# Kernel tuning notes

Hardware: AMD Instinct MI355X
Metric: run time of the kernel (lower is better)

## Reference

```python
import jax, jax.numpy as jnp
import numpy as np

B, N, X, Y, W1, W2 = 2, 6, 8, 8, 8, 8
DIM, HEADS, DHEAD = 128, 4, 32
HD = HEADS * DHEAD
EPS = 1e-5


def setup_inputs() -> dict:
    key = jax.random.key(0)
    ks = jax.random.split(key, 12)
    d = {}
    d['q'] = jax.random.normal(ks[0], (B, N, X, Y, W1, W2, DIM), jnp.float32)
    d['k'] = jax.random.normal(ks[1], (B, N, X, Y, W1, W2, DIM), jnp.float32)
    d['v'] = jax.random.normal(ks[2], (B, N, X, Y, W1, W2, DIM), jnp.float32)
    d['skip'] = jax.random.normal(ks[3], (B, X, Y, W1, W2, DIM), jnp.float32)
    d['head_gate'] = jax.random.uniform(ks[4], (HEADS,), jnp.float32, 0.5, 1.5)
    # LayerNorm affine params (slightly perturbed so grads are nontrivial)
    d['ln_q_w'] = 1.0 + 0.1 * jax.random.normal(ks[5], (DIM,), jnp.float32)
    d['ln_q_b'] = jnp.zeros((DIM,), jnp.float32)
    d['ln_k_w'] = 1.0 + 0.1 * jax.random.normal(ks[6], (DIM,), jnp.float32)
    d['ln_k_b'] = jnp.zeros((DIM,), jnp.float32)
    d['ln_v_w'] = 1.0 + 0.1 * jax.random.normal(ks[7], (DIM,), jnp.float32)
    d['ln_v_b'] = jnp.zeros((DIM,), jnp.float32)
    # Linear weights, stored as (in, out) so x @ w + b
    s = 0.02
    d['wq'] = s * jax.random.normal(ks[8], (DIM, HD), jnp.float32)
    d['bq'] = jnp.zeros((HD,), jnp.float32)
    d['wk'] = s * jax.random.normal(ks[9], (DIM, HD), jnp.float32)
    d['bk'] = jnp.zeros((HD,), jnp.float32)
    d['wv'] = s * jax.random.normal(ks[10], (DIM, HD), jnp.float32)
    d['bv'] = jnp.zeros((HD,), jnp.float32)
    d['wp'] = s * jax.random.normal(ks[11], (HD, DIM), jnp.float32)
    d['bp'] = jnp.zeros((DIM,), jnp.float32)
    return d


def _ln(x, w, b):
    mu = jnp.mean(x, axis=-1, keepdims=True)
    var = jnp.mean(jnp.square(x - mu), axis=-1, keepdims=True)
    return (x - mu) * jax.lax.rsqrt(var + EPS) * w + b


def _windows(t):
    # (b, n, x, y, w1, w2, d) -> (b, x*y, n*w1*w2, d)
    b, n, x, y, w1, w2, dd = t.shape
    return t.transpose(0, 2, 3, 1, 4, 5, 6).reshape(b, x * y, n * w1 * w2, dd)


def _heads(t):
    # (b, l, t, HEADS*DHEAD) -> (b, m, l, t, DHEAD)
    b, l, tt, _ = t.shape
    return t.reshape(b, l, tt, HEADS, DHEAD).transpose(0, 3, 1, 2, 4)


def reference(q, k, v, skip, head_gate,
              ln_q_w, ln_q_b, ln_k_w, ln_k_b, ln_v_w, ln_v_b,
              wq, bq, wk, bk, wv, bv, wp, bp):
    b, n, x, y, w1, w2, _ = q.shape
    scale = DHEAD ** -0.5
    qh = _heads(_ln(_windows(q), ln_q_w, ln_q_b) @ wq + bq) * scale
    kh = _heads(_ln(_windows(k), ln_k_w, ln_k_b) @ wk + bk)
    vh = _heads(_ln(_windows(v), ln_v_w, ln_v_b) @ wv + bv)
    # per-window attention: l = x*y windows, Q = K = n*w1*w2 tokens
    dot = jnp.einsum('bmlqd,bmlkd->bmlqk', qh, kh)
    dot = dot * head_gate[None, :, None, None, None]
    att = jax.nn.softmax(dot, axis=-1)
    a = jnp.einsum('bmlqk,bmlkd->bmlqd', att, vh)
    a = a.transpose(0, 2, 3, 1, 4).reshape(b, x * y, n * w1 * w2, HD)
    out = a.reshape(b, x, y, n, w1, w2, HD).transpose(0, 3, 1, 2, 4, 5, 6)
    z = out @ wp + bp          # (b, n, x, y, w1, w2, dim)
    z = jnp.mean(z, axis=1)    # mean over agents n
    return z + skip
```

## Files before the change

### kernel.cpp

```cpp
#include <hip/hip_runtime.h>
#include <hip/hip_bf16.h>
#include <cstddef>

#define NB     2
#define NA     6
#define NWIN   64
#define NTOK   384
#define DIM    128
#define NHEADS 4
#define DHEAD  32

typedef __attribute__((ext_vector_type(8))) short short8;
typedef __attribute__((ext_vector_type(4))) float f32x4;

__device__ __forceinline__ unsigned short f2bf(float f) {
    __hip_bfloat16 h = __float2bfloat16(f);
    return *reinterpret_cast<unsigned short*>(&h);
}
__device__ __forceinline__ float bf2f(unsigned short u) {
    union { unsigned int i; float f; } x; x.i = ((unsigned int)u) << 16; return x.f;
}

__global__ __launch_bounds__(256) void wconv_kernel(
    const float* __restrict__ wq, const float* __restrict__ wk,
    const float* __restrict__ wv, const float* __restrict__ gate,
    unsigned short* __restrict__ wt)
{
    const int e = blockIdx.x * 256 + threadIdx.x;
    const int mat = e >> 14, i = e & 16383;
    const int kk = i >> 7, c = i & 127;
    const float* src = (mat == 0) ? wq : (mat == 1) ? wk : wv;
    const float s = (mat == 0) ? (0.17677669529663687f * gate[c >> 5]) : 1.0f;
    wt[(mat << 14) + c * DIM + kk] = f2bf(src[i] * s);
}

__global__ __launch_bounds__(256, 4) void proj_kernel(
    const float* __restrict__ qx, const float* __restrict__ kx,
    const float* __restrict__ vx,
    const float* __restrict__ lnqw, const float* __restrict__ lnqb,
    const float* __restrict__ lnkw, const float* __restrict__ lnkb,
    const float* __restrict__ lnvw, const float* __restrict__ lnvb,
    const float* __restrict__ bq, const float* __restrict__ bk,
    const float* __restrict__ bv, const float* __restrict__ gate,
    const unsigned short* __restrict__ wt,
    unsigned short* __restrict__ qh, unsigned short* __restrict__ kh,
    unsigned short* __restrict__ vh)
{
    __shared__ unsigned short Wl[DIM * DIM];

    const int bid  = blockIdx.x;
    const int mode = bid / 768;
    const int rr   = bid - mode * 768;
    const int b = rr / 384, l = (rr / 6) % NWIN, n = rr % 6;

    const float* xin  = (mode == 0) ? qx : (mode == 1) ? kx : vx;
    const float* lw   = (mode == 0) ? lnqw : (mode == 1) ? lnkw : lnvw;
    const float* lb   = (mode == 0) ? lnqb : (mode == 1) ? lnkb : lnvb;
    const float* bias = (mode == 0) ? bq : (mode == 1) ? bk : bv;
    const unsigned short* wtm = wt + (mode << 14);
    unsigned short* outp = (mode == 0) ? qh : (mode == 1) ? kh : vh;

#pragma unroll
    for (int it = 0; it < 8; ++it) {
        const int e = it * 256 + threadIdx.x;
        const int col = e >> 4, k8 = (e & 15) * 8;
        *(short8*)&Wl[col * DIM + (k8 ^ ((col & 7) << 3))] =
            *(const short8*)&wtm[col * DIM + k8];
    }

    const int wv_ = threadIdx.x >> 6, lane = threadIdx.x & 63;
    const int g = lane >> 4, qc = lane & 15;
    const int T0 = wv_ * 16;

    const float* xp = xin + ((size_t)((b * NA + n) * NWIN + l) * 64 + T0 + qc) * DIM;
    float xv[4][8];
    float s = 0.f, s2 = 0.f;
#pragma unroll
    for (int c = 0; c < 4; ++c) {
        const float4 a0 = *(const float4*)(xp + c * 32 + 8 * g);
        const float4 a1 = *(const float4*)(xp + c * 32 + 8 * g + 4);
        xv[c][0] = a0.x; xv[c][1] = a0.y; xv[c][2] = a0.z; xv[c][3] = a0.w;
        xv[c][4] = a1.x; xv[c][5] = a1.y; xv[c][6] = a1.z; xv[c][7] = a1.w;
#pragma unroll
        for (int u = 0; u < 8; ++u) { s += xv[c][u]; s2 += xv[c][u] * xv[c][u]; }
    }
    s  += __shfl_xor(s, 16);  s  += __shfl_xor(s, 32);
    s2 += __shfl_xor(s2, 16); s2 += __shfl_xor(s2, 32);
    const float mu   = s * (1.0f / 128.0f);
    const float var  = s2 * (1.0f / 128.0f) - mu * mu;
    const float rsig = rsqrtf(var + 1e-5f);

    short8 af[4];
#pragma unroll
    for (int c = 0; c < 4; ++c) {
        const float4 w0 = *(const float4*)(lw + c * 32 + 8 * g);
        const float4 w1 = *(const float4*)(lw + c * 32 + 8 * g + 4);
        const float4 b0 = *(const float4*)(lb + c * 32 + 8 * g);
        const float4 b1 = *(const float4*)(lb + c * 32 + 8 * g + 4);
        af[c][0] = (short)f2bf((xv[c][0] - mu) * rsig * w0.x + b0.x);
        af[c][1] = (short)f2bf((xv[c][1] - mu) * rsig * w0.y + b0.y);
        af[c][2] = (short)f2bf((xv[c][2] - mu) * rsig * w0.z + b0.z);
        af[c][3] = (short)f2bf((xv[c][3] - mu) * rsig * w0.w + b0.w);
        af[c][4] = (short)f2bf((xv[c][4] - mu) * rsig * w1.x + b1.x);
        af[c][5] = (short)f2bf((xv[c][5] - mu) * rsig * w1.y + b1.y);
        af[c][6] = (short)f2bf((xv[c][6] - mu) * rsig * w1.z + b1.z);
        af[c][7] = (short)f2bf((xv[c][7] - mu) * rsig * w1.w + b1.w);
    }
    __syncthreads();

    const f32x4 z = {0.f, 0.f, 0.f, 0.f};
    const float gs = 0.17677669529663687f;
    const int swz = (qc & 7) << 3;

#pragma unroll
    for (int ct = 0; ct < 8; ++ct) {
        const int col = ct * 16 + qc;
        short8 wf[4];
#pragma unroll
        for (int c = 0; c < 4; ++c)
            wf[c] = *(const short8*)&Wl[col * DIM + ((c * 32 + 8 * g) ^ swz)];

        f32x4 acc = z;
        if (mode == 2) {
#pragma unroll
            for (int c = 0; c < 4; ++c)
                acc = __builtin_amdgcn_mfma_f32_16x16x32_bf16(af[c], wf[c], acc, 0, 0, 0);
            const int head = ct >> 1;
            const int d = (ct & 1) * 16 + qc;
            const float bb = bias[col];
            const size_t hb = (size_t)(b * NHEADS + head) * NWIN + l;
            ushort4 o;
            o.x = f2bf(acc[0] + bb); o.y = f2bf(acc[1] + bb);
            o.z = f2bf(acc[2] + bb); o.w = f2bf(acc[3] + bb);
            *(ushort4*)&outp[(hb * DHEAD + d) * NTOK + n * 64 + T0 + 4 * g] = o;
        } else {
#pragma unroll
            for (int c = 0; c < 4; ++c)
                acc = __builtin_amdgcn_mfma_f32_16x16x32_bf16(wf[c], af[c], acc, 0, 0, 0);
            const int head = ct >> 1;
            const int d0 = (ct & 1) * 16 + 4 * g;
            const float hs = (mode == 0) ? (gs * gate[head]) : 1.0f;
            const float4 b4 = *(const float4*)&bias[ct * 16 + 4 * g];
            const size_t hb = (size_t)(b * NHEADS + head) * NWIN + l;
            const int t = n * 64 + T0 + qc;
            ushort4 o;
            o.x = f2bf(acc[0] + b4.x * hs); o.y = f2bf(acc[1] + b4.y * hs);
            o.z = f2bf(acc[2] + b4.z * hs); o.w = f2bf(acc[3] + b4.w * hs);
            *(ushort4*)&outp[(hb * NTOK + t) * DHEAD + d0] = o;
        }
    }
}

__global__ __launch_bounds__(256) void attn_kernel(
    const unsigned short* __restrict__ qh, const unsigned short* __restrict__ kh,
    const unsigned short* __restrict__ vt, unsigned short* __restrict__ aout)
{
    __shared__ unsigned short P[4][3][16][40];

    const int tid  = threadIdx.x;
    const int w    = tid >> 6;
    const int lane = tid & 63;
    const int g    = lane >> 4;
    const int qc   = lane & 15;

    const int idx = blockIdx.x;
    const int b = idx >> 9, h = (idx >> 7) & 3, l = (idx >> 1) & 63, half = idx & 1;
    const size_t base = (size_t)((b * NHEADS + h) * NWIN + l) * (NTOK * DHEAD);
    const unsigned short* Qp = qh + base;
    const unsigned short* Kp = kh + base;
    const unsigned short* Vp = vt + base;

    short8 qf[3];
#pragma unroll
    for (int j = 0; j < 3; ++j)
        qf[j] = *(const short8*)(Qp + (size_t)(((half * 4 + w) * 3 + j) * 16 + qc) * DHEAD + 8 * g);

    f32x4 o0[3], o1[3];
    float psum[3];
    const f32x4 z = {0.f, 0.f, 0.f, 0.f};
#pragma unroll
    for (int j = 0; j < 3; ++j) { o0[j] = z; o1[j] = z; psum[j] = 0.f; }

    for (int kc = 0; kc < 12; ++kc) {
        const int k0 = kc * 32;
        const short8 ka0 = *(const short8*)(Kp + (size_t)(k0 + qc) * DHEAD + 8 * g);
        const short8 ka1 = *(const short8*)(Kp + (size_t)(k0 + 16 + qc) * DHEAD + 8 * g);
        const short8 vb0 = *(const short8*)(Vp + (size_t)qc * NTOK + k0 + 8 * g);
        const short8 vb1 = *(const short8*)(Vp + (size_t)(16 + qc) * NTOK + k0 + 8 * g);

#pragma unroll
        for (int j = 0; j < 3; ++j) {
            f32x4 s0 = __builtin_amdgcn_mfma_f32_16x16x32_bf16(ka0, qf[j], z, 0, 0, 0);
            f32x4 s1 = __builtin_amdgcn_mfma_f32_16x16x32_bf16(ka1, qf[j], z, 0, 0, 0);
            const float e0 = __expf(s0[0]), e1 = __expf(s0[1]), e2 = __expf(s0[2]), e3 = __expf(s0[3]);
            const float e4 = __expf(s1[0]), e5 = __expf(s1[1]), e6 = __expf(s1[2]), e7 = __expf(s1[3]);
            psum[j] += ((e0 + e1) + (e2 + e3)) + ((e4 + e5) + (e6 + e7));
            ushort4 pw0, pw1;
            pw0.x = f2bf(e0); pw0.y = f2bf(e1); pw0.z = f2bf(e2); pw0.w = f2bf(e3);
            pw1.x = f2bf(e4); pw1.y = f2bf(e5); pw1.z = f2bf(e6); pw1.w = f2bf(e7);
            *(ushort4*)&P[w][j][qc][4 * g]      = pw0;
            *(ushort4*)&P[w][j][qc][16 + 4 * g] = pw1;
        }
#pragma unroll
        for (int j = 0; j < 3; ++j) {
            const short8 pa = *(const short8*)&P[w][j][qc][8 * g];
            o0[j] = __builtin_amdgcn_mfma_f32_16x16x32_bf16(pa, vb0, o0[j], 0, 0, 0);
            o1[j] = __builtin_amdgcn_mfma_f32_16x16x32_bf16(pa, vb1, o1[j], 0, 0, 0);
        }
    }

#pragma unroll
    for (int j = 0; j < 3; ++j) {
        float ps = psum[j];
        ps += __shfl_xor(ps, 16);
        ps += __shfl_xor(ps, 32);
        const float inv = 1.0f / ps;
        const int q0 = ((half * 4 + w) * 3 + j) * 16;
        const size_t ob = ((size_t)(b * NWIN + l) * NTOK + q0) * (NHEADS * DHEAD) + h * DHEAD + qc;
#pragma unroll
        for (int r = 0; r < 4; ++r) {
            const float iv = __shfl(inv, 4 * g + r);
            aout[ob + (size_t)(4 * g + r) * (NHEADS * DHEAD)]      = f2bf(o0[j][r] * iv);
            aout[ob + (size_t)(4 * g + r) * (NHEADS * DHEAD) + 16] = f2bf(o1[j][r] * iv);
        }
    }
}

__global__ __launch_bounds__(256) void outproj_kernel(
    const unsigned short* __restrict__ a, const float* __restrict__ wp,
    const float* __restrict__ bp, const float* __restrict__ skip,
    float* __restrict__ outp)
{
    __shared__ float at[DIM * 68];
    __shared__ float wl[DIM * 64];

    const int tid = threadIdx.x;
    const int bid = blockIdx.x;
    const int b = bid >> 7, l = (bid >> 1) & 63, cg = bid & 1;
    const int c0 = cg * 64;

#pragma unroll
    for (int rep = 0; rep < 8; ++rep) {
        const int idx = rep * 256 + tid;
        const int row = idx >> 4, cc4 = idx & 15;
        *(float4*)&wl[row * 64 + cc4 * 4] = *(const float4*)&wp[row * 128 + c0 + cc4 * 4];
    }

    const size_t abase = (size_t)(b * NWIN + l) * NTOK * DIM;
#pragma unroll
    for (int r = 0; r < 32; ++r) {
        const int f = tid + 256 * r;
        const int w_ = f >> 7, d = f & 127;
        float s = 0.f;
#pragma unroll
        for (int n = 0; n < NA; ++n)
            s += bf2f(a[abase + (size_t)(n * 64 + w_) * DIM + d]);
        at[d * 68 + w_] = s * (1.0f / 6.0f);
    }
    __syncthreads();

    const int cx = tid & 15, ty = tid >> 4;
    float acc[4][4];
#pragma unroll
    for (int i = 0; i < 4; ++i)
#pragma unroll
        for (int j = 0; j < 4; ++j) acc[i][j] = 0.f;

#pragma unroll 4
    for (int i = 0; i < DIM; ++i) {
        const float4 wa = *(const float4*)&wl[i * 64 + 4 * cx];
        const float4 aa = *(const float4*)&at[i * 68 + 4 * ty];
        acc[0][0] += aa.x * wa.x; acc[0][1] += aa.x * wa.y; acc[0][2] += aa.x * wa.z; acc[0][3] += aa.x * wa.w;
        acc[1][0] += aa.y * wa.x; acc[1][1] += aa.y * wa.y; acc[1][2] += aa.y * wa.z; acc[1][3] += aa.y * wa.w;
        acc[2][0] += aa.z * wa.x; acc[2][1] += aa.z * wa.y; acc[2][2] += aa.z * wa.z; acc[2][3] += aa.z * wa.w;
        acc[3][0] += aa.w * wa.x; acc[3][1] += aa.w * wa.y; acc[3][2] += aa.w * wa.z; acc[3][3] += aa.w * wa.w;
    }

    const float4 bb = *(const float4*)&bp[c0 + 4 * cx];
#pragma unroll
    for (int u = 0; u < 4; ++u) {
        const int w_ = 4 * ty + u;
        const size_t oidx = ((size_t)(b * NWIN + l) * 64 + w_) * DIM + c0 + 4 * cx;
        const float4 sk = *(const float4*)&skip[oidx];
        float4 o;
        o.x = acc[u][0] + bb.x + sk.x;
        o.y = acc[u][1] + bb.y + sk.y;
        o.z = acc[u][2] + bb.z + sk.z;
        o.w = acc[u][3] + bb.w + sk.w;
        *(float4*)&outp[oidx] = o;
    }
}

extern "C" void kernel_launch(void* const* d_in, const int* in_sizes, int n_in,
                              void* d_out, int out_size, void* d_ws, size_t ws_size,
                              hipStream_t stream) {
    const float* q      = (const float*)d_in[0];
    const float* k      = (const float*)d_in[1];
    const float* v      = (const float*)d_in[2];
    const float* skip   = (const float*)d_in[3];
    const float* gate   = (const float*)d_in[4];
    const float* ln_q_w = (const float*)d_in[5];
    const float* ln_q_b = (const float*)d_in[6];
    const float* ln_k_w = (const float*)d_in[7];
    const float* ln_k_b = (const float*)d_in[8];
    const float* ln_v_w = (const float*)d_in[9];
    const float* ln_v_b = (const float*)d_in[10];
    const float* wq     = (const float*)d_in[11];
    const float* bq     = (const float*)d_in[12];
    const float* wk     = (const float*)d_in[13];
    const float* bk     = (const float*)d_in[14];
    const float* wv     = (const float*)d_in[15];
    const float* bv     = (const float*)d_in[16];
    const float* wp     = (const float*)d_in[17];
    const float* bp     = (const float*)d_in[18];
    float* outp = (float*)d_out;

    const size_t per = (size_t)NB * NHEADS * NWIN * NTOK * DHEAD;
    unsigned short* qh = (unsigned short*)d_ws;
    unsigned short* kh = qh + per;
    unsigned short* vh = kh + per;
    unsigned short* wt = vh + per;
    unsigned short* a  = wt + 3 * 16384;

    wconv_kernel<<<192, 256, 0, stream>>>(wq, wk, wv, gate, wt);
    proj_kernel<<<3 * NB * NWIN * NA, 256, 0, stream>>>(
        q, k, v, ln_q_w, ln_q_b, ln_k_w, ln_k_b, ln_v_w, ln_v_b,
        bq, bk, bv, gate, wt, qh, kh, vh);
    attn_kernel<<<NB * NHEADS * NWIN * 2, 256, 0, stream>>>(qh, kh, vh, a);
    outproj_kernel<<<NB * NWIN * 2, 256, 0, stream>>>(a, wp, bp, skip, outp);
}
```

Before: 80.61 us.

## Fold LayerNorm affine into projection weights and apply normalization post-GEMM

Folds the LayerNorm scale into the bf16 weight matrix and precomputes per-column sums of the weights against the LN weight and bias, so the projection runs on raw bf16 inputs. Mean and inverse std are applied after the MFMA as r*(acc - mu*s_c) + t_c. The proj kernel also grows to 384 threads, with each wave handling two 16-token tiles, which cuts the block count from 2304 to 768 and spreads each weight tile load over more rows. It adds a small wsum kernel. Feeding the unnormalized x into bf16 loses precision when the mean is large relative to the spread, and the subtraction after accumulation can cancel.

```diff
diff --git a/kernel.cpp b/kernel.cpp
--- a/kernel.cpp
+++ b/kernel.cpp
@@ -23,93 +23,126 @@
 
 __global__ __launch_bounds__(256) void wconv_kernel(
     const float* __restrict__ wq, const float* __restrict__ wk,
-    const float* __restrict__ wv, const float* __restrict__ gate,
+    const float* __restrict__ wv,
+    const float* __restrict__ lnqw, const float* __restrict__ lnkw,
+    const float* __restrict__ lnvw, const float* __restrict__ gate,
     unsigned short* __restrict__ wt)
 {
     const int e = blockIdx.x * 256 + threadIdx.x;
     const int mat = e >> 14, i = e & 16383;
     const int kk = i >> 7, c = i & 127;
     const float* src = (mat == 0) ? wq : (mat == 1) ? wk : wv;
+    const float* lnw = (mat == 0) ? lnqw : (mat == 1) ? lnkw : lnvw;
     const float s = (mat == 0) ? (0.17677669529663687f * gate[c >> 5]) : 1.0f;
-    wt[(mat << 14) + c * DIM + kk] = f2bf(src[i] * s);
-}
-
-__global__ __launch_bounds__(256, 4) void proj_kernel(
-    const float* __restrict__ qx, const float* __restrict__ kx,
-    const float* __restrict__ vx,
-    const float* __restrict__ lnqw, const float* __restrict__ lnqb,
-    const float* __restrict__ lnkw, const float* __restrict__ lnkb,
-    const float* __restrict__ lnvw, const float* __restrict__ lnvb,
+    wt[(mat << 14) + c * DIM + kk] = f2bf(src[i] * lnw[kk] * s);
+}
+
+__global__ __launch_bounds__(128) void wsum_kernel(
+    const float* __restrict__ wq, const float* __restrict__ wk,
+    const float* __restrict__ wv,
+    const float* __restrict__ lnqw, const float* __restrict__ lnkw,
+    const float* __restrict__ lnvw,
+    const float* __restrict__ lnqb, const float* __restrict__ lnkb,
+    const float* __restrict__ lnvb,
     const float* __restrict__ bq, const float* __restrict__ bk,
     const float* __restrict__ bv, const float* __restrict__ gate,
-    const unsigned short* __restrict__ wt,
-    unsigned short* __restrict__ qh, unsigned short* __restrict__ kh,
-    unsigned short* __restrict__ vh)
-{
-    __shared__ unsigned short Wl[DIM * DIM];
-
-    const int bid  = blockIdx.x;
-    const int mode = bid / 768;
-    const int rr   = bid - mode * 768;
-    const int b = rr / 384, l = (rr / 6) % NWIN, n = rr % 6;
-
-    const float* xin  = (mode == 0) ? qx : (mode == 1) ? kx : vx;
-    const float* lw   = (mode == 0) ? lnqw : (mode == 1) ? lnkw : lnvw;
-    const float* lb   = (mode == 0) ? lnqb : (mode == 1) ? lnkb : lnvb;
-    const float* bias = (mode == 0) ? bq : (mode == 1) ? bk : bv;
-    const unsigned short* wtm = wt + (mode << 14);
-    unsigned short* outp = (mode == 0) ? qh : (mode == 1) ? kh : vh;
-
-#pragma unroll
-    for (int it = 0; it < 8; ++it) {
-        const int e = it * 256 + threadIdx.x;
-        const int col = e >> 4, k8 = (e & 15) * 8;
-        *(short8*)&Wl[col * DIM + (k8 ^ ((col & 7) << 3))] =
-            *(const short8*)&wtm[col * DIM + k8];
-    }
-
-    const int wv_ = threadIdx.x >> 6, lane = threadIdx.x & 63;
-    const int g = lane >> 4, qc = lane & 15;
-    const int T0 = wv_ * 16;
-
-    const float* xp = xin + ((size_t)((b * NA + n) * NWIN + l) * 64 + T0 + qc) * DIM;
-    float xv[4][8];
+    float* __restrict__ scol, float* __restrict__ tcol)
+{
+    const int mat = blockIdx.x, c = threadIdx.x;
+    const float* src  = (mat == 0) ? wq : (mat == 1) ? wk : wv;
+    const float* lnw  = (mat == 0) ? lnqw : (mat == 1) ? lnkw : lnvw;
+    const float* lnb  = (mat == 0) ? lnqb : (mat == 1) ? lnkb : lnvb;
+    const float* bias = (mat == 0) ? bq : (mat == 1) ? bk : bv;
+    float s = 0.f, t = 0.f;
+    for (int k = 0; k < DIM; ++k) {
+        const float w = src[k * DIM + c];
+        s += lnw[k] * w;
+        t += lnb[k] * w;
+    }
+    const float qs = (mat == 0) ? (0.17677669529663687f * gate[c >> 5]) : 1.0f;
+    scol[mat * DIM + c] = s * qs;
+    tcol[mat * DIM + c] = (t + bias[c]) * qs;
+}
+
+__device__ __forceinline__ void load_unit(
+    const float* __restrict__ xp, int g, short8* __restrict__ af,
+    float& mu, float& rsig)
+{
     float s = 0.f, s2 = 0.f;
 #pragma unroll
     for (int c = 0; c < 4; ++c) {
         const float4 a0 = *(const float4*)(xp + c * 32 + 8 * g);
         const float4 a1 = *(const float4*)(xp + c * 32 + 8 * g + 4);
-        xv[c][0] = a0.x; xv[c][1] = a0.y; xv[c][2] = a0.z; xv[c][3] = a0.w;
-        xv[c][4] = a1.x; xv[c][5] = a1.y; xv[c][6] = a1.z; xv[c][7] = a1.w;
-#pragma unroll
-        for (int u = 0; u < 8; ++u) { s += xv[c][u]; s2 += xv[c][u] * xv[c][u]; }
+        short8 o;
+        o[0] = (short)f2bf(a0.x); o[1] = (short)f2bf(a0.y);
+        o[2] = (short)f2bf(a0.z); o[3] = (short)f2bf(a0.w);
+        o[4] = (short)f2bf(a1.x); o[5] = (short)f2bf(a1.y);
+        o[6] = (short)f2bf(a1.z); o[7] = (short)f2bf(a1.w);
+        af[c] = o;
+        s  += ((a0.x + a0.y) + (a0.z + a0.w)) + ((a1.x + a1.y) + (a1.z + a1.w));
+        s2 += ((a0.x * a0.x + a0.y * a0.y) + (a0.z * a0.z + a0.w * a0.w))
+            + ((a1.x * a1.x + a1.y * a1.y) + (a1.z * a1.z + a1.w * a1.w));
     }
     s  += __shfl_xor(s, 16);  s  += __shfl_xor(s, 32);
     s2 += __shfl_xor(s2, 16); s2 += __shfl_xor(s2, 32);
-    const float mu   = s * (1.0f / 128.0f);
-    const float var  = s2 * (1.0f / 128.0f) - mu * mu;
-    const float rsig = rsqrtf(var + 1e-5f);
-
-    short8 af[4];
-#pragma unroll
-    for (int c = 0; c < 4; ++c) {
-        const float4 w0 = *(const float4*)(lw + c * 32 + 8 * g);
-        const float4 w1 = *(const float4*)(lw + c * 32 + 8 * g + 4);
-        const float4 b0 = *(const float4*)(lb + c * 32 + 8 * g);
-        const float4 b1 = *(const float4*)(lb + c * 32 + 8 * g + 4);
-        af[c][0] = (short)f2bf((xv[c][0] - mu) * rsig * w0.x + b0.x);
-        af[c][1] = (short)f2bf((xv[c][1] - mu) * rsig * w0.y + b0.y);
-        af[c][2] = (short)f2bf((xv[c][2] - mu) * rsig * w0.z + b0.z);
-        af[c][3] = (short)f2bf((xv[c][3] - mu) * rsig * w0.w + b0.w);
-        af[c][4] = (short)f2bf((xv[c][4] - mu) * rsig * w1.x + b1.x);
-        af[c][5] = (short)f2bf((xv[c][5] - mu) * rsig * w1.y + b1.y);
-        af[c][6] = (short)f2bf((xv[c][6] - mu) * rsig * w1.z + b1.z);
-        af[c][7] = (short)f2bf((xv[c][7] - mu) * rsig * w1.w + b1.w);
-    }
+    mu   = s * (1.0f / 128.0f);
+    rsig = rsqrtf(s2 * (1.0f / 128.0f) - mu * mu + 1e-5f);
+}
+
+__global__ __launch_bounds__(384) void proj_kernel(
+    const float* __restrict__ qx, const float* __restrict__ kx,
+    const float* __restrict__ vx,
+    const unsigned short* __restrict__ wt,
+    const float* __restrict__ scol, const float* __restrict__ tcol,
+    unsigned short* __restrict__ qh, unsigned short* __restrict__ kh,
+    unsigned short* __restrict__ vh)
+{
+    __shared__ unsigned short Wl[DIM * DIM];
+
+    const int bid  = blockIdx.x;
+    const int mode = bid >> 8;
+    const int rr   = bid & 255;
+    const int b = rr >> 7, l = (rr >> 1) & 63, ng = rr & 1;
+
+    const float* xin = (mode == 0) ? qx : (mode == 1) ? kx : vx;
+    const unsigned short* wtm = wt + (mode << 14);
+    const float* sc = scol + mode * DIM;
+    const float* tc = tcol + mode * DIM;
+    unsigned short* outp = (mode == 0) ? qh : (mode == 1) ? kh : vh;
+
+#pragma unroll
+    for (int it = 0; it < 6; ++it) {
+        const int e = it * 384 + threadIdx.x;
+        if (e < 2048) {
+            const int col = e >> 4, k8 = (e & 15) * 8;
+            *(short8*)&Wl[col * DIM + (k8 ^ ((col & 7) << 3))] =
+                *(const short8*)&wtm[col * DIM + k8];
+        }
+    }
+
+    const int wv_ = threadIdx.x / 64;
+    const int lane = threadIdx.x & 63;
+    const int g = lane >> 4, qc = lane & 15;
+    const int n  = ng * 3 + (wv_ >> 1);
+    const int t0 = (wv_ & 1) * 32;
+
+    const float* xp = xin + ((size_t)((b * NA + n) * NWIN + l) * 64 + t0 + qc) * DIM;
+    short8 af0[4], af1[4];
+    float mu0, rs0, mu1, rs1;
+    load_unit(xp, g, af0, mu0, rs0);
+    load_unit(xp + 16 * DIM, g, af1, mu1, rs1);
     __syncthreads();
 
+    float m0[4], r0[4], m1[4], r1[4];
+    if (mode == 2) {
+#pragma unroll
+        for (int r = 0; r < 4; ++r) {
+            m0[r] = __shfl(mu0, 4 * g + r); r0[r] = __shfl(rs0, 4 * g + r);
+            m1[r] = __shfl(mu1, 4 * g + r); r1[r] = __shfl(rs1, 4 * g + r);
+        }
+    }
+
     const f32x4 z = {0.f, 0.f, 0.f, 0.f};
-    const float gs = 0.17677669529663687f;
     const int swz = (qc & 7) << 3;
 
 #pragma unroll
@@ -120,33 +153,52 @@
         for (int c = 0; c < 4; ++c)
             wf[c] = *(const short8*)&Wl[col * DIM + ((c * 32 + 8 * g) ^ swz)];
 
-        f32x4 acc = z;
+        f32x4 a0 = z, a1 = z;
         if (mode == 2) {
 #pragma unroll
-            for (int c = 0; c < 4; ++c)
-                acc = __builtin_amdgcn_mfma_f32_16x16x32_bf16(af[c], wf[c], acc, 0, 0, 0);
+            for (int c = 0; c < 4; ++c) {
+                a0 = __builtin_amdgcn_mfma_f32_16x16x32_bf16(af0[c], wf[c], a0, 0, 0, 0);
+                a1 = __builtin_amdgcn_mfma_f32_16x16x32_bf16(af1[c], wf[c], a1, 0, 0, 0);
+            }
+            const float s_c = sc[col], t_c = tc[col];
             const int head = ct >> 1;
             const int d = (ct & 1) * 16 + qc;
-            const float bb = bias[col];
-            const size_t hb = (size_t)(b * NHEADS + head) * NWIN + l;
+            const size_t rowb = ((size_t)(b * NHEADS + head) * NWIN + l) * DHEAD + d;
+            unsigned short* dst = outp + rowb * NTOK + n * 64 + t0 + 4 * g;
             ushort4 o;
-            o.x = f2bf(acc[0] + bb); o.y = f2bf(acc[1] + bb);
-            o.z = f2bf(acc[2] + bb); o.w = f2bf(acc[3] + bb);
-            *(ushort4*)&outp[(hb * DHEAD + d) * NTOK + n * 64 + T0 + 4 * g] = o;
+            o.x = f2bf(r0[0] * (a0[0] - m0[0] * s_c) + t_c);
+            o.y = f2bf(r0[1] * (a0[1] - m0[1] * s_c) + t_c);
+            o.z = f2bf(r0[2] * (a0[2] - m0[2] * s_c) + t_c);
+            o.w = f2bf(r0[3] * (a0[3] - m0[3] * s_c) + t_c);
+            *(ushort4*)&dst[0] = o;
+            o.x = f2bf(r1[0] * (a1[0] - m1[0] * s_c) + t_c);
+            o.y = f2bf(r1[1] * (a1[1] - m1[1] * s_c) + t_c);
+            o.z = f2bf(r1[2] * (a1[2] - m1[2] * s_c) + t_c);
+            o.w = f2bf(r1[3] * (a1[3] - m1[3] * s_c) + t_c);
+            *(ushort4*)&dst[16] = o;
         } else {
 #pragma unroll
-            for (int c = 0; c < 4; ++c)
-                acc = __builtin_amdgcn_mfma_f32_16x16x32_bf16(wf[c], af[c], acc, 0, 0, 0);
+            for (int c = 0; c < 4; ++c) {
+                a0 = __builtin_amdgcn_mfma_f32_16x16x32_bf16(wf[c], af0[c], a0, 0, 0, 0);
+                a1 = __builtin_amdgcn_mfma_f32_16x16x32_bf16(wf[c], af1[c], a1, 0, 0, 0);
+            }
             const int head = ct >> 1;
             const int d0 = (ct & 1) * 16 + 4 * g;
-            const float hs = (mode == 0) ? (gs * gate[head]) : 1.0f;
-            const float4 b4 = *(const float4*)&bias[ct * 16 + 4 * g];
+            const float4 s4 = *(const float4*)&sc[ct * 16 + 4 * g];
+            const float4 t4 = *(const float4*)&tc[ct * 16 + 4 * g];
             const size_t hb = (size_t)(b * NHEADS + head) * NWIN + l;
-            const int t = n * 64 + T0 + qc;
+            unsigned short* dst = outp + (hb * NTOK + n * 64 + t0 + qc) * DHEAD + d0;
             ushort4 o;
-            o.x = f2bf(acc[0] + b4.x * hs); o.y = f2bf(acc[1] + b4.y * hs);
-            o.z = f2bf(acc[2] + b4.z * hs); o.w = f2bf(acc[3] + b4.w * hs);
-            *(ushort4*)&outp[(hb * NTOK + t) * DHEAD + d0] = o;
+            o.x = f2bf(rs0 * (a0[0] - mu0 * s4.x) + t4.x);
+            o.y = f2bf(rs0 * (a0[1] - mu0 * s4.y) + t4.y);
+            o.z = f2bf(rs0 * (a0[2] - mu0 * s4.z) + t4.z);
+            o.w = f2bf(rs0 * (a0[3] - mu0 * s4.w) + t4.w);
+            *(ushort4*)&dst[0] = o;
+            o.x = f2bf(rs1 * (a1[0] - mu1 * s4.x) + t4.x);
+            o.y = f2bf(rs1 * (a1[1] - mu1 * s4.y) + t4.y);
+            o.z = f2bf(rs1 * (a1[2] - mu1 * s4.z) + t4.z);
+            o.w = f2bf(rs1 * (a1[3] - mu1 * s4.w) + t4.w);
+            *(ushort4*)&dst[16 * DHEAD] = o;
         }
     }
 }
@@ -321,11 +373,14 @@
     unsigned short* vh = kh + per;
     unsigned short* wt = vh + per;
     unsigned short* a  = wt + 3 * 16384;
-
-    wconv_kernel<<<192, 256, 0, stream>>>(wq, wk, wv, gate, wt);
-    proj_kernel<<<3 * NB * NWIN * NA, 256, 0, stream>>>(
-        q, k, v, ln_q_w, ln_q_b, ln_k_w, ln_k_b, ln_v_w, ln_v_b,
-        bq, bk, bv, gate, wt, qh, kh, vh);
+    float* scol = (float*)(a + per);
+    float* tcol = scol + 3 * DIM;
+
+    wconv_kernel<<<192, 256, 0, stream>>>(wq, wk, wv, ln_q_w, ln_k_w, ln_v_w, gate, wt);
+    wsum_kernel<<<3, 128, 0, stream>>>(wq, wk, wv, ln_q_w, ln_k_w, ln_v_w,
+                                       ln_q_b, ln_k_b, ln_v_b, bq, bk, bv, gate,
+                                       scol, tcol);
+    proj_kernel<<<768, 384, 0, stream>>>(q, k, v, wt, scol, tcol, qh, kh, vh);
     attn_kernel<<<NB * NHEADS * NWIN * 2, 256, 0, stream>>>(qh, kh, vh, a);
     outproj_kernel<<<NB * NWIN * 2, 256, 0, stream>>>(a, wp, bp, skip, outp);
 }
```

After: 77.22 us. 4.2% less time.
